# Kernel optimization log

Hardware: AMD Instinct MI355X
Metric: run time of the kernel (lower is better)

Reference implementation:

```python
import jax, jax.numpy as jnp
import numpy as np
from jax import lax

N = 8388608
NG = 1024
TAU = 0.1
GAMMA = 0.05
MAX_ITERS = 30
EPS = 1e-9


def setup_inputs() -> dict:
    key = jax.random.key(0)
    k1, k2, k3 = jax.random.split(key, 3)
    y_raw = jax.random.uniform(k1, (N,), dtype=jnp.float32)
    y_real = jax.random.uniform(k2, (N,), dtype=jnp.float32)
    group_ids = jax.random.randint(k3, (N,), 0, NG, dtype=jnp.int32)
    return {"y_raw": y_raw, "y_real": y_real, "group_ids": group_ids, "n_groups": NG}


def reference(y_raw, y_real, group_ids, n_groups):
    y_real = jnp.maximum(y_real, EPS)
    l = (1.0 - TAU) * y_real          # per-element lower box bound
    u = (1.0 + TAU) * y_real          # per-element upper box bound
    y_clipped = jnp.clip(y_raw, l, u)
    w = 1.0 / jnp.maximum(y_real, 1e-9)

    seg_sum = lambda v: jax.ops.segment_sum(v, group_ids, num_segments=n_groups)

    n_g = seg_sum(jnp.ones_like(y_raw))            # [G] group sizes
    L = (1.0 - GAMMA) * n_g
    U = (1.0 + GAMMA) * n_g
    S0 = seg_sum(w * y_clipped)                    # [G] ratio sums at alpha=0
    feasible = (S0 >= L) & (S0 <= U)

    # per-group bracketing interval for alpha
    alo = jax.ops.segment_min((l - y_raw) * w, group_ids, num_segments=n_groups) - 1.0
    ahi = jax.ops.segment_max((u - y_raw) * w, group_ids, num_segments=n_groups) + 1.0
    nonempty = n_g > 0
    alo = jnp.where(nonempty, alo, 0.0)            # guard empty groups (inf/-inf)
    ahi = jnp.where(nonempty, ahi, 0.0)
    T = jnp.where(S0 < L, L, U)                    # [G] bisection target

    def step(carry, _):
        lo, hi, _ = carry
        mid = 0.5 * (lo + hi)                                    # [G]
        y_mid = jnp.clip(y_raw + mid[group_ids] / w, l, u)       # [N]
        Smid = seg_sum(w * y_mid)                                # [G]
        lo = jnp.where(Smid < T, mid, lo)
        hi = jnp.where(Smid >= T, mid, hi)
        return (lo, hi, mid), None

    (lo, hi, mid), _ = lax.scan(step, (alo, ahi, alo), None, length=MAX_ITERS)
    y_bis = jnp.clip(y_raw + mid[group_ids] / w, l, u)           # last iterate y_mid
    return jnp.where(feasible[group_ids], y_clipped, y_bis)
```

## Files before the change

kernel.cpp:

```cpp
#include <hip/hip_runtime.h>

#define NGROUPS  1024
#define EPSF     1e-9f
#define MAX_ITERS 30
#define CNT_SHIFT 18
#define SUM_MASK  0x3FFFFu
#define QSCALE    128.0f
#define QINV      (1.0f / 128.0f)
#define SBLK 512
#define PTILE 2
#define PERBLK (SBLK * PTILE)
#define NSHADOW 32

typedef float vfloat4 __attribute__((ext_vector_type(4)));

__device__ __forceinline__ unsigned enc_f(float f) {
    unsigned u = __float_as_uint(f);
    return (u & 0x80000000u) ? ~u : (u | 0x80000000u);
}
__device__ __forceinline__ float dec_f(unsigned e) {
    unsigned u = (e & 0x80000000u) ? (e ^ 0x80000000u) : ~e;
    return __uint_as_float(u);
}

__global__ __launch_bounds__(NGROUPS) void k_init(unsigned* gpack) {
#pragma unroll
    for (int c = 0; c < NSHADOW; ++c) gpack[c * NGROUPS + threadIdx.x] = 0u;
}

__device__ __forceinline__ void stats4(float4 yr, float4 ye, int4 gg,
                                       unsigned* s_pk, float4* __restrict__ out4,
                                       int idx) {
    float yrs[4] = { yr.x, yr.y, yr.z, yr.w };
    float yes[4] = { ye.x, ye.y, ye.z, ye.w };
    int   gs[4]  = { gg.x, gg.y, gg.z, gg.w };
    float oc[4];
#pragma unroll
    for (int j = 0; j < 4; ++j) {
        float yraw = yrs[j];
        float yrc  = fmaxf(yes[j], EPSF);
        float l = 0.9f * yrc;
        float u = 1.1f * yrc;
        float yclip = fminf(fmaxf(yraw, l), u);
        oc[j] = yclip;
        float s = yclip / yrc;
        unsigned pk = (1u << CNT_SHIFT)
                    + __float2uint_rn((s - 0.9f) * QSCALE);
        atomicAdd(&s_pk[gs[j]], pk);
    }
    vfloat4 o = { oc[0], oc[1], oc[2], oc[3] };
    __builtin_nontemporal_store(o, (vfloat4*)&out4[idx]);
}

template <bool EXACT>
__global__ __launch_bounds__(SBLK, 8) void k_stats(const float4* __restrict__ yraw4,
                                                   const float4* __restrict__ yreal4,
                                                   const int4*   __restrict__ gid4,
                                                   float4*       __restrict__ out4,
                                                   unsigned* gpack, int n4) {
    __shared__ unsigned s_pk[NGROUPS];
    int t = threadIdx.x;
    int base = blockIdx.x * PERBLK + t;

    s_pk[t] = 0u; s_pk[t + SBLK] = 0u;
    __syncthreads();

    if (EXACT) {
        float4 yr0, yr1, ye0, ye1;
        int4   gg0, gg1;
        yr0 = yraw4[base];            yr1 = yraw4[base + SBLK];
        ye0 = yreal4[base];           ye1 = yreal4[base + SBLK];
        gg0 = gid4[base];             gg1 = gid4[base + SBLK];

        stats4(yr0, ye0, gg0, s_pk, out4, base);
        stats4(yr1, ye1, gg1, s_pk, out4, base + SBLK);
    } else {
#pragma unroll
        for (int k = 0; k < PTILE; ++k) {
            int i = base + k * SBLK;
            if (i >= n4) continue;
            float4 a = yraw4[i], b = yreal4[i];
            int4 g4 = gid4[i];
            stats4(a, b, g4, s_pk, out4, i);
        }
    }
    __syncthreads();
    unsigned lo = s_pk[2 * t], hi = s_pk[2 * t + 1];
    if (lo | hi) {
        unsigned* gp = gpack + (blockIdx.x & (NSHADOW - 1)) * NGROUPS;
        unsigned long long pair = ((unsigned long long)hi << 32) | (unsigned long long)lo;
        atomicAdd((unsigned long long*)&gp[2 * t], pair);
    }
}

__global__ __launch_bounds__(NGROUPS) void k_group(const unsigned* gpack,
                                                   unsigned* feas, float* gT,
                                                   unsigned* gmn, unsigned* gmx,
                                                   unsigned* gbase, unsigned* gcur,
                                                   unsigned* gcnt, unsigned* total) {
    __shared__ unsigned s_scan[NGROUPS];
    int g = threadIdx.x;
    unsigned c = 0u, q = 0u;
#pragma unroll
    for (int s = 0; s < NSHADOW; ++s) {
        unsigned pk = gpack[s * NGROUPS + g];
        c += pk >> CNT_SHIFT;
        q += pk & SUM_MASK;
    }
    float nf = (float)c;
    float S0 = 0.9f * nf + (float)q * QINV;
    float L = 0.95f * nf;
    float U = 1.05f * nf;
    unsigned f = (S0 >= L && S0 <= U) ? 1u : 0u;
    feas[g] = f;
    gT[g]   = (S0 < L) ? L : U;
    gcnt[g] = c;
    gmn[g]  = 0xFFFFFFFFu;
    gmx[g]  = 0u;

    unsigned v = f ? 0u : c;
    s_scan[g] = v;
    for (int off = 1; off < NGROUPS; off <<= 1) {
        __syncthreads();
        unsigned tmp = (g >= off) ? s_scan[g - off] : 0u;
        __syncthreads();
        s_scan[g] += tmp;
    }
    __syncthreads();
    unsigned incl = s_scan[g];
    unsigned base = incl - v;
    gbase[g] = base;
    gcur[g]  = base;
    if (g == NGROUPS - 1) *total = incl;
}

__global__ __launch_bounds__(256) void k_mmc(const float4* __restrict__ yraw4,
                                             const float4* __restrict__ yreal4,
                                             const int4*   __restrict__ gid4,
                                             const unsigned* __restrict__ feas,
                                             unsigned* gcur, const unsigned* total,
                                             unsigned* gmn, unsigned* gmx,
                                             unsigned* cidx, unsigned* cgid,
                                             unsigned capacity, int n4) {
    if (*total == 0u) return;
    __shared__ unsigned s_feas[NGROUPS];
    __shared__ unsigned s_mn[NGROUPS];
    __shared__ unsigned s_mx[NGROUPS];
    for (int g = threadIdx.x; g < NGROUPS; g += blockDim.x) {
        s_feas[g] = feas[g]; s_mn[g] = 0xFFFFFFFFu; s_mx[g] = 0u;
    }
    __syncthreads();
    int stride = gridDim.x * blockDim.x;
    for (int i = blockIdx.x * blockDim.x + threadIdx.x; i < n4; i += stride) {
        int4 gg = gid4[i];
        int gs[4] = { gg.x, gg.y, gg.z, gg.w };
        bool any = !s_feas[gs[0]] || !s_feas[gs[1]] || !s_feas[gs[2]] || !s_feas[gs[3]];
        if (!any) continue;
        float4 yr = yraw4[i];
        float4 ye = yreal4[i];
        float yrs[4] = { yr.x, yr.y, yr.z, yr.w };
        float yes[4] = { ye.x, ye.y, ye.z, ye.w };
#pragma unroll
        for (int j = 0; j < 4; ++j) {
            int g = gs[j];
            if (s_feas[g]) continue;
            float yraw = yrs[j];
            float yrc  = fmaxf(yes[j], EPSF);
            float l = 0.9f * yrc;
            float u = 1.1f * yrc;
            float w = 1.0f / yrc;
            float a0 = (l - yraw) * w;
            float a1 = (u - yraw) * w;
            atomicMin(&s_mn[g], enc_f(a0));
            atomicMax(&s_mx[g], enc_f(a1));
            unsigned pos = atomicAdd(&gcur[g], 1u);
            if (pos < capacity) {
                cidx[pos] = (unsigned)(4 * i + j);
                cgid[pos] = (unsigned)g;
            }
        }
    }
    __syncthreads();
    for (int g = threadIdx.x; g < NGROUPS; g += blockDim.x) {
        if (!s_feas[g]) {
            atomicMin(&gmn[g], s_mn[g]);
            atomicMax(&gmx[g], s_mx[g]);
        }
    }
}

#define CAPC 8064
__global__ __launch_bounds__(256) void k_bisect(const float* __restrict__ y_raw,
                                                const float* __restrict__ y_real,
                                                const unsigned* feas,
                                                const unsigned* gcnt,
                                                const unsigned* gbase, const float* gT,
                                                const unsigned* gmn, const unsigned* gmx,
                                                const unsigned* __restrict__ cidx,
                                                float* __restrict__ out,
                                                unsigned capacity) {
    int g = blockIdx.x;
    if (feas[g]) return;
    __shared__ float2 cache[CAPC];
    __shared__ double s_part[4];
    __shared__ float  s_mid;
    unsigned base = gbase[g];
    unsigned cnt  = gcnt[g];
    if (base >= capacity) cnt = 0;
    else if (cnt > capacity - base) cnt = capacity - base;
    int t = threadIdx.x;
    for (unsigned i = t; i < cnt && i < CAPC; i += 256u) {
        unsigned idx = cidx[base + i];
        cache[i] = make_float2(y_raw[idx], y_real[idx]);
    }
    __syncthreads();
    float lo = dec_f(gmn[g]) - 1.0f;
    float hi = dec_f(gmx[g]) + 1.0f;
    float T  = gT[g];
    for (int it = 0; it < MAX_ITERS; ++it) {
        if (t == 0) s_mid = 0.5f * (lo + hi);
        __syncthreads();
        float m = s_mid;
        double part = 0.0;
        for (unsigned i = t; i < cnt; i += 256u) {
            float yraw, ye;
            if (i < CAPC) { float2 v = cache[i]; yraw = v.x; ye = v.y; }
            else { unsigned idx = cidx[base + i]; yraw = y_raw[idx]; ye = y_real[idx]; }
            float yrc = fmaxf(ye, EPSF);
            float l = 0.9f * yrc;
            float u = 1.1f * yrc;
            float w = 1.0f / yrc;
            float ym = fminf(fmaxf(yraw + m / w, l), u);
            part += (double)(w * ym);
        }
#pragma unroll
        for (int off = 32; off > 0; off >>= 1) part += __shfl_down(part, off, 64);
        if ((t & 63) == 0) s_part[t >> 6] = part;
        __syncthreads();
        if (t == 0) {
            float Smid = (float)(s_part[0] + s_part[1] + s_part[2] + s_part[3]);
            if (Smid < T) lo = m; else hi = m;
        }
        __syncthreads();
    }
    float m = s_mid;
    for (unsigned i = t; i < cnt; i += 256u) {
        unsigned idx = cidx[base + i];
        float yraw, ye;
        if (i < CAPC) { float2 v = cache[i]; yraw = v.x; ye = v.y; }
        else { yraw = y_raw[idx]; ye = y_real[idx]; }
        float yrc = fmaxf(ye, EPSF);
        float l = 0.9f * yrc;
        float u = 1.1f * yrc;
        float w = 1.0f / yrc;
        out[idx] = fminf(fmaxf(yraw + m / w, l), u);
    }
}

extern "C" void kernel_launch(void* const* d_in, const int* in_sizes, int n_in,
                              void* d_out, int out_size, void* d_ws, size_t ws_size,
                              hipStream_t stream) {
    const float* y_raw  = (const float*)d_in[0];
    const float* y_real = (const float*)d_in[1];
    const int*   gid    = (const int*)d_in[2];
    float* out = (float*)d_out;
    const int n  = in_sizes[0];
    const int n4 = n / 4;

    char* ws = (char*)d_ws;
    unsigned* gpack  = (unsigned*)(ws + 0);
    unsigned* gmn    = (unsigned*)(ws + 131072);
    unsigned* gmx    = (unsigned*)(ws + 135168);
    unsigned* feas   = (unsigned*)(ws + 139264);
    float*    gT     = (float*)(ws + 143360);
    unsigned* gbase  = (unsigned*)(ws + 147456);
    unsigned* gcur   = (unsigned*)(ws + 151552);
    unsigned* gcnt   = (unsigned*)(ws + 155648);
    unsigned* total  = (unsigned*)(ws + 159744);
    unsigned* cidx   = (unsigned*)(ws + 163840);
    size_t cap64 = (ws_size > 163840) ? (ws_size - 163840) / 8 : 0;
    if (cap64 > (size_t)n) cap64 = (size_t)n;
    unsigned capacity = (unsigned)cap64;
    unsigned* cgid = cidx + capacity;

    k_init<<<1, NGROUPS, 0, stream>>>(gpack);
    if (n4 % PERBLK == 0) {
        k_stats<true><<<n4 / PERBLK, SBLK, 0, stream>>>(
            (const float4*)y_raw, (const float4*)y_real, (const int4*)gid,
            (float4*)out, gpack, n4);
    } else {
        k_stats<false><<<(n4 + PERBLK - 1) / PERBLK, SBLK, 0, stream>>>(
            (const float4*)y_raw, (const float4*)y_real, (const int4*)gid,
            (float4*)out, gpack, n4);
    }
    k_group<<<1, NGROUPS, 0, stream>>>(gpack, feas, gT, gmn, gmx, gbase, gcur,
                                       gcnt, total);
    k_mmc<<<512, 256, 0, stream>>>((const float4*)y_raw, (const float4*)y_real,
                                   (const int4*)gid, feas, gcur, total,
                                   gmn, gmx, cidx, cgid, capacity, n4);
    k_bisect<<<NGROUPS, 256, 0, stream>>>(y_raw, y_real, feas, gcnt, gbase, gT,
                                          gmn, gmx, cidx, out, capacity);
}
```

Before: 146.1 us.

## Fuse init and group-summary kernels into stats kernel via last-block completion

Removes the separate zeroing kernel and the single-block group kernel. The last block of k_stats to finish, found with an atomic done counter, now computes the group feasibility, targets and prefix scan. Counters reset themselves by subtracting a reference value P and then writing P back, which avoids a clearing pass each call. This relies on the workspace already holding consistent values on the first call. The stats block size also doubles to 1024 threads, which changes occupancy and register pressure under the existing launch bounds.

```diff
diff --git a/kernel.cpp b/kernel.cpp
--- a/kernel.cpp
+++ b/kernel.cpp
@@ -7,7 +7,7 @@
 #define SUM_MASK  0x3FFFFu
 #define QSCALE    128.0f
 #define QINV      (1.0f / 128.0f)
-#define SBLK 512
+#define SBLK 1024
 #define PTILE 2
 #define PERBLK (SBLK * PTILE)
 #define NSHADOW 32
@@ -21,11 +21,6 @@
 __device__ __forceinline__ float dec_f(unsigned e) {
     unsigned u = (e & 0x80000000u) ? (e ^ 0x80000000u) : ~e;
     return __uint_as_float(u);
-}
-
-__global__ __launch_bounds__(NGROUPS) void k_init(unsigned* gpack) {
-#pragma unroll
-    for (int c = 0; c < NSHADOW; ++c) gpack[c * NGROUPS + threadIdx.x] = 0u;
 }
 
 __device__ __forceinline__ void stats4(float4 yr, float4 ye, int4 gg,
@@ -57,21 +52,25 @@
                                                    const float4* __restrict__ yreal4,
                                                    const int4*   __restrict__ gid4,
                                                    float4*       __restrict__ out4,
-                                                   unsigned* gpack, int n4) {
+                                                   unsigned* gpack, unsigned* done,
+                                                   const unsigned* gref,
+                                                   unsigned* feas, float* gT,
+                                                   unsigned* gmn, unsigned* gmx,
+                                                   unsigned* gbase, unsigned* gcur,
+                                                   unsigned* gcnt, unsigned* total,
+                                                   int n4) {
     __shared__ unsigned s_pk[NGROUPS];
+    __shared__ unsigned s_last;
     int t = threadIdx.x;
     int base = blockIdx.x * PERBLK + t;
 
-    s_pk[t] = 0u; s_pk[t + SBLK] = 0u;
+    s_pk[t] = 0u;
     __syncthreads();
 
     if (EXACT) {
-        float4 yr0, yr1, ye0, ye1;
-        int4   gg0, gg1;
-        yr0 = yraw4[base];            yr1 = yraw4[base + SBLK];
-        ye0 = yreal4[base];           ye1 = yreal4[base + SBLK];
-        gg0 = gid4[base];             gg1 = gid4[base + SBLK];
-
+        float4 yr0 = yraw4[base], yr1 = yraw4[base + SBLK];
+        float4 ye0 = yreal4[base], ye1 = yreal4[base + SBLK];
+        int4   gg0 = gid4[base],  gg1 = gid4[base + SBLK];
         stats4(yr0, ye0, gg0, s_pk, out4, base);
         stats4(yr1, ye1, gg1, s_pk, out4, base + SBLK);
     } else {
@@ -85,25 +84,35 @@
         }
     }
     __syncthreads();
-    unsigned lo = s_pk[2 * t], hi = s_pk[2 * t + 1];
-    if (lo | hi) {
-        unsigned* gp = gpack + (blockIdx.x & (NSHADOW - 1)) * NGROUPS;
-        unsigned long long pair = ((unsigned long long)hi << 32) | (unsigned long long)lo;
-        atomicAdd((unsigned long long*)&gp[2 * t], pair);
-    }
-}
-
-__global__ __launch_bounds__(NGROUPS) void k_group(const unsigned* gpack,
-                                                   unsigned* feas, float* gT,
-                                                   unsigned* gmn, unsigned* gmx,
-                                                   unsigned* gbase, unsigned* gcur,
-                                                   unsigned* gcnt, unsigned* total) {
-    __shared__ unsigned s_scan[NGROUPS];
-    int g = threadIdx.x;
+    if (t < NGROUPS / 2) {
+        unsigned lo = s_pk[2 * t], hi = s_pk[2 * t + 1];
+        if (lo | hi) {
+            unsigned* gp = gpack + (blockIdx.x & (NSHADOW - 1)) * NGROUPS;
+            unsigned long long pair =
+                ((unsigned long long)hi << 32) | (unsigned long long)lo;
+            atomicAdd((unsigned long long*)&gp[2 * t], pair);
+        }
+    }
+
+    __threadfence();
+    if (t == 0) {
+        unsigned P = __hip_atomic_load(gref, __ATOMIC_RELAXED,
+                                       __HIP_MEMORY_SCOPE_AGENT);
+        unsigned old = atomicAdd(done, 1u);
+        s_last = ((old - P) == gridDim.x - 1u) ? 1u : 0u;
+    }
+    __syncthreads();
+    if (!s_last) return;
+
+    __threadfence();
+    unsigned P = __hip_atomic_load(gref, __ATOMIC_RELAXED,
+                                   __HIP_MEMORY_SCOPE_AGENT);
+    int g = t;
     unsigned c = 0u, q = 0u;
 #pragma unroll
     for (int s = 0; s < NSHADOW; ++s) {
-        unsigned pk = gpack[s * NGROUPS + g];
+        unsigned pk = __hip_atomic_load(&gpack[s * NGROUPS + g], __ATOMIC_RELAXED,
+                                        __HIP_MEMORY_SCOPE_AGENT) - P;
         c += pk >> CNT_SHIFT;
         q += pk & SUM_MASK;
     }
@@ -118,7 +127,9 @@
     gmn[g]  = 0xFFFFFFFFu;
     gmx[g]  = 0u;
 
+    unsigned* s_scan = s_pk;
     unsigned v = f ? 0u : c;
+    __syncthreads();
     s_scan[g] = v;
     for (int off = 1; off < NGROUPS; off <<= 1) {
         __syncthreads();
@@ -128,10 +139,13 @@
     }
     __syncthreads();
     unsigned incl = s_scan[g];
-    unsigned base = incl - v;
-    gbase[g] = base;
-    gcur[g]  = base;
+    unsigned b = incl - v;
+    gbase[g] = b;
+    gcur[g]  = b;
     if (g == NGROUPS - 1) *total = incl;
+
+    for (int i = t; i < NSHADOW * NGROUPS; i += SBLK) gpack[i] = P;
+    if (t == 0) *done = P;
 }
 
 __global__ __launch_bounds__(256) void k_mmc(const float4* __restrict__ yraw4,
@@ -269,32 +283,33 @@
 
     char* ws = (char*)d_ws;
     unsigned* gpack  = (unsigned*)(ws + 0);
-    unsigned* gmn    = (unsigned*)(ws + 131072);
-    unsigned* gmx    = (unsigned*)(ws + 135168);
-    unsigned* feas   = (unsigned*)(ws + 139264);
-    float*    gT     = (float*)(ws + 143360);
-    unsigned* gbase  = (unsigned*)(ws + 147456);
-    unsigned* gcur   = (unsigned*)(ws + 151552);
-    unsigned* gcnt   = (unsigned*)(ws + 155648);
-    unsigned* total  = (unsigned*)(ws + 159744);
-    unsigned* cidx   = (unsigned*)(ws + 163840);
-    size_t cap64 = (ws_size > 163840) ? (ws_size - 163840) / 8 : 0;
+    unsigned* done   = (unsigned*)(ws + 131072);
+    const unsigned* gref = (const unsigned*)(ws + 131136);
+    unsigned* gmn    = (unsigned*)(ws + 135168);
+    unsigned* gmx    = (unsigned*)(ws + 139264);
+    unsigned* feas   = (unsigned*)(ws + 143360);
+    float*    gT     = (float*)(ws + 147456);
+    unsigned* gbase  = (unsigned*)(ws + 151552);
+    unsigned* gcur   = (unsigned*)(ws + 155648);
+    unsigned* gcnt   = (unsigned*)(ws + 159744);
+    unsigned* total  = (unsigned*)(ws + 163840);
+    unsigned* cidx   = (unsigned*)(ws + 167936);
+    size_t cap64 = (ws_size > 167936) ? (ws_size - 167936) / 8 : 0;
     if (cap64 > (size_t)n) cap64 = (size_t)n;
     unsigned capacity = (unsigned)cap64;
     unsigned* cgid = cidx + capacity;
 
-    k_init<<<1, NGROUPS, 0, stream>>>(gpack);
     if (n4 % PERBLK == 0) {
         k_stats<true><<<n4 / PERBLK, SBLK, 0, stream>>>(
             (const float4*)y_raw, (const float4*)y_real, (const int4*)gid,
-            (float4*)out, gpack, n4);
+            (float4*)out, gpack, done, gref, feas, gT, gmn, gmx,
+            gbase, gcur, gcnt, total, n4);
     } else {
         k_stats<false><<<(n4 + PERBLK - 1) / PERBLK, SBLK, 0, stream>>>(
             (const float4*)y_raw, (const float4*)y_real, (const int4*)gid,
-            (float4*)out, gpack, n4);
-    }
-    k_group<<<1, NGROUPS, 0, stream>>>(gpack, feas, gT, gmn, gmx, gbase, gcur,
-                                       gcnt, total);
+            (float4*)out, gpack, done, gref, feas, gT, gmn, gmx,
+            gbase, gcur, gcnt, total, n4);
+    }
     k_mmc<<<512, 256, 0, stream>>>((const float4*)y_raw, (const float4*)y_real,
                                    (const int4*)gid, feas, gcur, total,
                                    gmn, gmx, cidx, cgid, capacity, n4);
```

After: 582.2 us. 299% more time.
